# Kernel tuning notes

Hardware: AMD Instinct MI355X
Metric: run time of the kernel (lower is better)

The kernel has to match this reference:

```python
import jax, jax.numpy as jnp
import numpy as np

B, N, K = 2, 8192, 16          # batch, points, ED_nsample
SA_C, DG_C = 128, 1024         # SA_conv_out, DG_conv_out
CAT_C = SA_C + SA_C // 4 + 4   # 164 channels into head


def _conv1(W, b, x):
    # 1x1 Conv1d: W [out,in], x [B,in,N]
    return jnp.einsum('oc,bcn->bon', W, x) + b[None, :, None]


def _bn_relu(x, g, be):
    # BatchNorm1d (training-mode batch stats) + ReLU, x [B,C,N]
    m = x.mean(axis=(0, 2), keepdims=True)
    v = x.var(axis=(0, 2), keepdims=True)
    return jax.nn.relu((x - m) * jax.lax.rsqrt(v + 1e-5) * g[None, :, None] + be[None, :, None])


def setup_inputs() -> dict:
    key = jax.random.key(0)
    ks = jax.random.split(key, 32)
    w = lambda k, s: jax.random.normal(k, s, jnp.float32) * 0.05
    p = {}
    p['pointcloud'] = jax.random.normal(ks[0], (B, N, 3), jnp.float32)
    p['h1'] = jax.random.normal(ks[1], (B, SA_C, N), jnp.float32)
    p['h2'] = jax.random.normal(ks[2], (B, DG_C, N), jnp.float32)
    p['numpoints'] = N
    # DG head convs 1024->256->64->32
    p['DG_w1'], p['DG_b1'] = w(ks[3], (256, DG_C)), jnp.zeros(256, jnp.float32)
    p['DG_g1'], p['DG_be1'] = jnp.ones(256, jnp.float32), jnp.zeros(256, jnp.float32)
    p['DG_w2'], p['DG_b2'] = w(ks[4], (64, 256)), jnp.zeros(64, jnp.float32)
    p['DG_g2'], p['DG_be2'] = jnp.ones(64, jnp.float32), jnp.zeros(64, jnp.float32)
    p['DG_w3'], p['DG_b3'] = w(ks[5], (SA_C // 4, 64)), jnp.zeros(SA_C // 4, jnp.float32)
    p['DG_g3'], p['DG_be3'] = jnp.ones(SA_C // 4, jnp.float32), jnp.zeros(SA_C // 4, jnp.float32)
    # ED MLP 3->4->4
    p['ED_w1'], p['ED_b1'] = w(ks[6], (3, 4)), jnp.zeros(4, jnp.float32)
    p['ED_w2'], p['ED_b2'] = w(ks[7], (4, 4)), jnp.zeros(4, jnp.float32)
    # head convs 164->512->256->128
    p['C_w1'], p['C_b1'] = w(ks[8], (512, CAT_C)), jnp.zeros(512, jnp.float32)
    p['C_g1'], p['C_be1'] = jnp.ones(512, jnp.float32), jnp.zeros(512, jnp.float32)
    p['C_w2'], p['C_b2'] = w(ks[9], (256, 512)), jnp.zeros(256, jnp.float32)
    p['C_g2'], p['C_be2'] = jnp.ones(256, jnp.float32), jnp.zeros(256, jnp.float32)
    p['C_w3'], p['C_b3'] = w(ks[10], (128, 256)), jnp.zeros(128, jnp.float32)
    p['C_g3'], p['C_be3'] = jnp.ones(128, jnp.float32), jnp.zeros(128, jnp.float32)
    return p


def reference(pointcloud, h1, h2, numpoints,
              DG_w1, DG_b1, DG_g1, DG_be1, DG_w2, DG_b2, DG_g2, DG_be2,
              DG_w3, DG_b3, DG_g3, DG_be3,
              ED_w1, ED_b1, ED_w2, ED_b2,
              C_w1, C_b1, C_g1, C_be1, C_w2, C_b2, C_g2, C_be2,
              C_w3, C_b3, C_g3, C_be3):
    xyz = pointcloud[..., :3]
    # DG branch head
    h2p = _bn_relu(_conv1(DG_w1, DG_b1, h2), DG_g1, DG_be1)
    h2p = _bn_relu(_conv1(DG_w2, DG_b2, h2p), DG_g2, DG_be2)
    h2p = _bn_relu(_conv1(DG_w3, DG_b3, h2p), DG_g3, DG_be3)
    # ED branch: brute-force knn on squared distances
    sq = jnp.sum(xyz * xyz, axis=-1)                               # [B,N]
    d = sq[:, :, None] + sq[:, None, :] - 2.0 * jnp.einsum('bnd,bmd->bnm', xyz, xyz)
    _, idx = jax.lax.top_k(-d, K)                                  # [B,N,K]
    nbr = jax.vmap(lambda pts, i: pts[i])(xyz, idx)                # [B,N,K,3]
    c = nbr - nbr.mean(axis=2, keepdims=True)
    cov = jnp.einsum('bnkd,bnke->bnde', c, c) / K                  # [B,N,3,3]
    ev = jnp.linalg.eigvalsh(cov)                                  # [B,N,3] ascending
    h3 = jax.nn.relu(ev @ ED_w1 + ED_b1) @ ED_w2 + ED_b2           # [B,N,4]
    # fuse and head
    z = jnp.concatenate([h1, h2p, jnp.transpose(h3, (0, 2, 1))], axis=1)
    z = _bn_relu(_conv1(C_w1, C_b1, z), C_g1, C_be1)
    z = _bn_relu(_conv1(C_w2, C_b2, z), C_g2, C_be2)
    z = _bn_relu(_conv1(C_w3, C_b3, z), C_g3, C_be3)
    return xyz, z
```

## Files before the change

### kernel.cpp

```cpp
#include <hip/hip_runtime.h>

#define NPTS 8192
#define BATCH 2

typedef __attribute__((ext_vector_type(8))) __bf16 bf16x8;
typedef __attribute__((ext_vector_type(4))) float f32x4;
typedef unsigned int u32;

__device__ inline unsigned short f2bf(float x) {
    unsigned u = __float_as_uint(x);
    u += 0x7fffu + ((u >> 16) & 1u);
    return (unsigned short)(u >> 16);
}
__device__ inline unsigned pack32(float d, unsigned idx) {
    unsigned u = __float_as_uint(d);
    u ^= ((unsigned)((int)u >> 31)) | 0x80000000u;
    return (u & 0xFFFFE000u) | idx;
}
__device__ inline unsigned bitonic64u(unsigned key, int lane) {
#pragma unroll
    for (int k = 2; k <= 64; k <<= 1) {
#pragma unroll
        for (int j = k >> 1; j > 0; j >>= 1) {
            unsigned o = __shfl_xor(key, j, 64);
            bool tmin = (((lane & k) == 0) == ((lane & j) == 0));
            key = ((o < key) == tmin) ? o : key;
        }
    }
    return key;
}
__device__ inline void ins16(unsigned& key, unsigned c, int lane) {
    unsigned prev = __shfl_up(key, 1, 64);
    if (lane == 0) prev = 0u;
    unsigned mx = prev > c ? prev : c;
    key = mx < key ? mx : key;
}
__device__ inline float distf(float4 q, float4 p) {
    return fmaf(-2.f, fmaf(q.z, p.z, fmaf(q.y, p.y, q.x * p.x)), q.w + p.w);
}

__global__ __launch_bounds__(256) void prep_presplit(
    const float* __restrict__ pc, float* __restrict__ oxyz, float4* __restrict__ pq,
    const float* __restrict__ W0, const float* __restrict__ W1,
    const float* __restrict__ W2, const float* __restrict__ W3,
    const float* __restrict__ W4, const float* __restrict__ W5,
    unsigned short* __restrict__ wsp) {
    int bx = blockIdx.x, tid = threadIdx.x;
    if (bx < 64) {
        int t = bx * 256 + tid;
        float x = pc[t * 3 + 0], y = pc[t * 3 + 1], z = pc[t * 3 + 2];
        oxyz[t * 3 + 0] = x; oxyz[t * 3 + 1] = y; oxyz[t * 3 + 2] = z;
        pq[t] = make_float4(x, y, z, fmaf(z, z, fmaf(y, y, x * x)));
        return;
    }
    int pb = bx - 64;
    const float* W; int O, C, OP; size_t off; int base;
    if (pb < 1024)      { W = W0; O = 256; C = 1024; OP = 256; off = 0;       base = 0; }
    else if (pb < 1152) { W = W1; O =  64; C =  256; OP = 128; off = 524288;  base = 1024; }
    else if (pb < 1184) { W = W2; O =  32; C =   64; OP = 128; off = 589824;  base = 1152; }
    else if (pb < 1568) { W = W3; O = 512; C =  164; OP = 512; off = 606208;  base = 1184; }
    else if (pb < 2080) { W = W4; O = 256; C =  512; OP = 256; off = 802816;  base = 1568; }
    else                { W = W5; O = 128; C =  256; OP = 128; off = 1064960; base = 2080; }
    unsigned short* dst = wsp + off;
    int t = (pb - base) * 256 + tid;
    int kk = t & 31;
    int o = (t >> 5) % OP;
    int kt = t / (OP * 32);
    int c = kt * 32 + kk;
    float x = (o < O && c < C) ? W[o * C + c] : 0.f;
    unsigned short hb = f2bf(x);
    float hf = __uint_as_float((unsigned)hb << 16);
    unsigned short lb = f2bf(x - hf);
    int s = kk >> 3, pos = kk & 7;
    int sst = s ^ ((o >> 1) & 3);
    dst[((size_t)(kt * 2) * OP + o) * 32 + sst * 8 + pos] = hb;
    dst[((size_t)(kt * 2 + 1) * OP + o) * 32 + sst * 8 + pos] = lb;
}

template <int MODE>
__global__ __launch_bounds__(256, 2) void mfma_gemm(
    const unsigned short* __restrict__ Wsp, const float* __restrict__ bias,
    const float* __restrict__ X, float* __restrict__ out,
    int O, int C, int OP, int nK,
    const float2* __restrict__ stats,
    const float* __restrict__ h1, const float* __restrict__ h3,
    const float2* __restrict__ stats3) {
    const int N = NPTS;
    int tid = threadIdx.x;
    int lane = tid & 63, w = tid >> 6;
    int wm = w >> 1, wn = w & 1;
    int b = blockIdx.z, n0 = blockIdx.x * 64, o0 = blockIdx.y * 128;
    int n = n0 + lane;

    __shared__ __align__(16) unsigned char lds[26624];
    unsigned char* WHp = lds;
    unsigned char* WLp = lds + 8192;
    unsigned char* XHp = lds + 16384;
    unsigned char* XLp = lds + 21504;

    f32x4 acc[4][2];
#pragma unroll
    for (int i = 0; i < 4; ++i)
#pragma unroll
        for (int j = 0; j < 2; ++j) acc[i][j] = (f32x4){0.f, 0.f, 0.f, 0.f};

    float xcur[8], xnxt[8];

    auto loadx = [&](int kt, float (&dst)[8]) {
#pragma unroll
        for (int i = 0; i < 8; ++i) {
            int c = kt * 32 + w * 8 + i;
            float x = 0.f;
            if (MODE == 0 || MODE == 1) {
                if (c < C) x = X[((size_t)(b * C + c)) * N + n];
            } else {
                if (c < 128)       x = h1[((size_t)(b * 128 + c)) * N + n];
                else if (c < 160)  x = X[((size_t)(b * 32 + (c - 128))) * N + n];
                else if (c < 164)  x = h3[((size_t)(b * 4 + (c - 160))) * N + n];
            }
            dst[i] = x;
        }
    };

    loadx(0, xcur);
    for (int kt = 0; kt < nK; ++kt) {
        int c0 = kt * 32;
#pragma unroll
        for (int comp = 0; comp < 2; ++comp) {
            const unsigned short* gb = Wsp + ((size_t)(kt * 2 + comp) * OP + o0) * 32;
            unsigned char* lb = comp ? WLp : WHp;
#pragma unroll
            for (int i = 0; i < 2; ++i) {
                int chunk = w + i * 4;
                __builtin_amdgcn_global_load_lds(
                    (const __attribute__((address_space(1))) u32*)(gb + chunk * 512 + lane * 8),
                    (__attribute__((address_space(3))) u32*)(lb + chunk * 1024),
                    16, 0, 0);
            }
        }
        {
            union { bf16x8 s; unsigned short u[8]; } hh, ll;
#pragma unroll
            for (int i = 0; i < 8; ++i) {
                int c = c0 + w * 8 + i;
                float x = xcur[i];
                if (MODE == 1) {
                    if (c < C) {
                        float2 st = stats[c];
                        x = fmaxf(fmaf(x, st.x, st.y), 0.f);
                    }
                } else if (MODE == 2) {
                    if (c >= 128 && c < 160) {
                        float2 st = stats3[c - 128];
                        x = fmaxf(fmaf(x, st.x, st.y), 0.f);
                    }
                }
                unsigned short hb = f2bf(x);
                float hf = __uint_as_float((unsigned)hb << 16);
                unsigned short lb = f2bf(x - hf);
                hh.u[i] = hb; ll.u[i] = lb;
            }
            *(bf16x8*)(XHp + lane * 80 + w * 16) = hh.s;
            *(bf16x8*)(XLp + lane * 80 + w * 16) = ll.s;
        }
        if (kt + 1 < nK) loadx(kt + 1, xnxt);
        __syncthreads();
        {
            int koff = (lane >> 4) * 16;
            int rb = wn * 32 + (lane & 15);
            bf16x8 bh[2], bl[2];
#pragma unroll
            for (int ni = 0; ni < 2; ++ni) {
                bh[ni] = *(const bf16x8*)(XHp + (rb + ni * 16) * 80 + koff);
                bl[ni] = *(const bf16x8*)(XLp + (rb + ni * 16) * 80 + koff);
            }
#pragma unroll
            for (int mi = 0; mi < 4; ++mi) {
                int ra = wm * 64 + mi * 16 + (lane & 15);
                int sw = koff ^ ((((unsigned)ra >> 1) & 3) * 16);
                bf16x8 ah = *(const bf16x8*)(WHp + ra * 64 + sw);
                bf16x8 al = *(const bf16x8*)(WLp + ra * 64 + sw);
#pragma unroll
                for (int ni = 0; ni < 2; ++ni) {
                    acc[mi][ni] = __builtin_amdgcn_mfma_f32_16x16x32_bf16(ah, bh[ni], acc[mi][ni], 0, 0, 0);
                    acc[mi][ni] = __builtin_amdgcn_mfma_f32_16x16x32_bf16(ah, bl[ni], acc[mi][ni], 0, 0, 0);
                    acc[mi][ni] = __builtin_amdgcn_mfma_f32_16x16x32_bf16(al, bh[ni], acc[mi][ni], 0, 0, 0);
                }
            }
        }
        __syncthreads();
        if (kt + 1 < nK) {
#pragma unroll
            for (int i = 0; i < 8; ++i) xcur[i] = xnxt[i];
        }
    }
    int col = lane & 15, rq = lane >> 4;
#pragma unroll
    for (int mi = 0; mi < 4; ++mi) {
#pragma unroll
        for (int j = 0; j < 4; ++j) {
            int o = o0 + wm * 64 + mi * 16 + rq * 4 + j;
            if (o < O) {
                float bs = bias[o];
                float* po = out + ((size_t)(b * O + o)) * N + n0 + wn * 32 + col;
#pragma unroll
                for (int ni = 0; ni < 2; ++ni) po[ni * 16] = acc[mi][ni][j] + bs;
            }
        }
    }
}

__global__ __launch_bounds__(256) void stats_kernel(const float* __restrict__ X,
                                                    const float* __restrict__ g,
                                                    const float* __restrict__ be,
                                                    float2* __restrict__ st, int C) {
    const int N = NPTS;
    int c = blockIdx.x;
    int tid = threadIdx.x;
    float s1 = 0.f, s2 = 0.f;
    for (int b = 0; b < BATCH; ++b) {
        const float* p = X + (size_t)(b * C + c) * N;
        for (int n = tid * 4; n < N; n += 1024) {
            float4 v = *(const float4*)(p + n);
            s1 += v.x + v.y + v.z + v.w;
            s2 += v.x * v.x + v.y * v.y + v.z * v.z + v.w * v.w;
        }
    }
    __shared__ float r1[256], r2[256];
    r1[tid] = s1; r2[tid] = s2;
    __syncthreads();
    for (int off = 128; off > 0; off >>= 1) {
        if (tid < off) { r1[tid] += r1[tid + off]; r2[tid] += r2[tid + off]; }
        __syncthreads();
    }
    if (tid == 0) {
        float inv = 1.f / (BATCH * N);
        float m = r1[0] * inv;
        float var = r2[0] * inv - m * m;
        float sc = g[c] * rsqrtf(var + 1e-5f);
        st[c] = make_float2(sc, be[c] - m * sc);
    }
}

__global__ __launch_bounds__(256) void stats_final_kernel(const float* __restrict__ X,
                                                          const float* __restrict__ g,
                                                          const float* __restrict__ be,
                                                          float* __restrict__ outz) {
    const int N = NPTS;
    const int C = 128;
    int c = blockIdx.x;
    int tid = threadIdx.x;
    float s1 = 0.f, s2 = 0.f;
    for (int b = 0; b < BATCH; ++b) {
        const float* p = X + (size_t)(b * C + c) * N;
        for (int n = tid * 4; n < N; n += 1024) {
            float4 v = *(const float4*)(p + n);
            s1 += v.x + v.y + v.z + v.w;
            s2 += v.x * v.x + v.y * v.y + v.z * v.z + v.w * v.w;
        }
    }
    __shared__ float r1[256], r2[256];
    __shared__ float2 stv;
    r1[tid] = s1; r2[tid] = s2;
    __syncthreads();
    for (int off = 128; off > 0; off >>= 1) {
        if (tid < off) { r1[tid] += r1[tid + off]; r2[tid] += r2[tid + off]; }
        __syncthreads();
    }
    if (tid == 0) {
        float inv = 1.f / (BATCH * N);
        float m = r1[0] * inv;
        float var = r2[0] * inv - m * m;
        float sc = g[c] * rsqrtf(var + 1e-5f);
        stv = make_float2(sc, be[c] - m * sc);
    }
    __syncthreads();
    float2 s = stv;
    for (int b = 0; b < BATCH; ++b) {
        const float* p = X + (size_t)(b * C + c) * N;
        float* q = outz + (size_t)(b * C + c) * N;
        for (int nn = tid * 4; nn < N; nn += 1024) {
            float4 v = *(const float4*)(p + nn);
            v.x = fmaxf(fmaf(v.x, s.x, s.y), 0.f);
            v.y = fmaxf(fmaf(v.y, s.x, s.y), 0.f);
            v.z = fmaxf(fmaf(v.z, s.x, s.y), 0.f);
            v.w = fmaxf(fmaf(v.w, s.x, s.y), 0.f);
            *(float4*)(q + nn) = v;
        }
    }
}

__global__ __launch_bounds__(256) void knn_eig_kernel(
    const float4* __restrict__ pq,
    const float* __restrict__ ew1, const float* __restrict__ eb1,
    const float* __restrict__ ew2, const float* __restrict__ eb2,
    float* __restrict__ h3) {
    int wv = threadIdx.x >> 6;
    int lane = threadIdx.x & 63;
    int sg = blockIdx.x * 4 + wv;
    int b = sg >> 12;
    int iloc = (sg & 4095) << 1;
    const float4* pqb = pq + (size_t)b * NPTS;
    float4 Q0 = pqb[iloc + 0], Q1 = pqb[iloc + 1];

    float4 p = pqb[lane];
    unsigned k0 = bitonic64u(pack32(distf(Q0, p), lane), lane);
    unsigned k1 = bitonic64u(pack32(distf(Q1, p), lane), lane);
    unsigned tk0 = (unsigned)__builtin_amdgcn_readlane((int)k0, 15);
    unsigned tk1 = (unsigned)__builtin_amdgcn_readlane((int)k1, 15);

    float4 A = pqb[64 + lane];
    float4 B = pqb[128 + lane];
    for (int it = 1; it + 1 < 128; it += 2) {
        int tbA = it * 64, tbB = tbA + 64;
        int t3 = (it + 3 < 128) ? it + 3 : 0;
        float4 Cx = pqb[(it + 2) * 64 + lane];
        float4 Dx = pqb[t3 * 64 + lane];
        unsigned cA0 = pack32(distf(Q0, A), tbA + lane);
        unsigned cA1 = pack32(distf(Q1, A), tbA + lane);
        unsigned cB0 = pack32(distf(Q0, B), tbB + lane);
        unsigned cB1 = pack32(distf(Q1, B), tbB + lane);
        unsigned long long mA0 = __ballot(cA0 < tk0), mB0 = __ballot(cB0 < tk0);
        unsigned long long mA1 = __ballot(cA1 < tk1), mB1 = __ballot(cB1 < tk1);
        if (mA0 | mA1 | mB0 | mB1) {
            while (mA0) {
                int L = __ffsll((long long)mA0) - 1; mA0 &= mA0 - 1;
                ins16(k0, (unsigned)__builtin_amdgcn_readlane((int)cA0, L), lane);
            }
            while (mB0) {
                int L = __ffsll((long long)mB0) - 1; mB0 &= mB0 - 1;
                ins16(k0, (unsigned)__builtin_amdgcn_readlane((int)cB0, L), lane);
            }
            while (mA1) {
                int L = __ffsll((long long)mA1) - 1; mA1 &= mA1 - 1;
                ins16(k1, (unsigned)__builtin_amdgcn_readlane((int)cA1, L), lane);
            }
            while (mB1) {
                int L = __ffsll((long long)mB1) - 1; mB1 &= mB1 - 1;
                ins16(k1, (unsigned)__builtin_amdgcn_readlane((int)cB1, L), lane);
            }
            tk0 = (unsigned)__builtin_amdgcn_readlane((int)k0, 15);
            tk1 = (unsigned)__builtin_amdgcn_readlane((int)k1, 15);
        }
        A = Cx; B = Dx;
    }
    {
        int tbA = 127 * 64;
        unsigned cA0 = pack32(distf(Q0, A), tbA + lane);
        unsigned cA1 = pack32(distf(Q1, A), tbA + lane);
        unsigned long long mA0 = __ballot(cA0 < tk0);
        unsigned long long mA1 = __ballot(cA1 < tk1);
        while (mA0) {
            int L = __ffsll((long long)mA0) - 1; mA0 &= mA0 - 1;
            ins16(k0, (unsigned)__builtin_amdgcn_readlane((int)cA0, L), lane);
        }
        while (mA1) {
            int L = __ffsll((long long)mA1) - 1; mA1 &= mA1 - 1;
            ins16(k1, (unsigned)__builtin_amdgcn_readlane((int)cA1, L), lane);
        }
    }

    int g = lane >> 4, r = lane & 15;
    unsigned j0 = ((unsigned)__shfl((int)k0, r, 64)) & 8191u;
    unsigned j1 = ((unsigned)__shfl((int)k1, r, 64)) & 8191u;
    unsigned nj = ((g & 1) == 0) ? j0 : j1;

    float4 nb = pqb[nj];
    float sx = nb.x, sy = nb.y, sz = nb.z;
#pragma unroll
    for (int m = 1; m < 16; m <<= 1) {
        sx += __shfl_xor(sx, m, 64);
        sy += __shfl_xor(sy, m, 64);
        sz += __shfl_xor(sz, m, 64);
    }
    const float i16 = 1.f / 16.f;
    float cx = nb.x - sx * i16, cy = nb.y - sy * i16, cz = nb.z - sz * i16;
    float xx = cx * cx, xy = cx * cy, xz = cx * cz, yy = cy * cy, yz = cy * cz, zz = cz * cz;
#pragma unroll
    for (int m = 1; m < 16; m <<= 1) {
        xx += __shfl_xor(xx, m, 64); xy += __shfl_xor(xy, m, 64); xz += __shfl_xor(xz, m, 64);
        yy += __shfl_xor(yy, m, 64); yz += __shfl_xor(yz, m, 64); zz += __shfl_xor(zz, m, 64);
    }
    float a11 = xx * i16, a12 = xy * i16, a13 = xz * i16,
          a22 = yy * i16, a23 = yz * i16, a33 = zz * i16;
    float q = (a11 + a22 + a33) * (1.f / 3.f);
    float p1 = a12 * a12 + a13 * a13 + a23 * a23;
    float b11 = a11 - q, b22 = a22 - q, b33 = a33 - q;
    float p2 = b11 * b11 + b22 * b22 + b33 * b33 + 2.f * p1;
    float pr = sqrtf(p2 * (1.f / 6.f));
    float ipv = (p2 > 1e-32f) ? (1.f / pr) : 0.f;
    float detB = b11 * (b22 * b33 - a23 * a23) - a12 * (a12 * b33 - a23 * a13) +
                 a13 * (a12 * a23 - b22 * a13);
    float r3 = 0.5f * detB * ipv * ipv * ipv;
    r3 = fminf(1.f, fmaxf(-1.f, r3));
    float phi = acosf(r3) * (1.f / 3.f);
    float e1 = q + 2.f * pr * cosf(phi);
    float e3 = q + 2.f * pr * cosf(phi + 2.0943951023931953f);
    float e2 = 3.f * q - e1 - e3;
    float ev0 = e3, ev1 = e2, ev2 = e1;
    float h[4], o[4];
#pragma unroll
    for (int kk = 0; kk < 4; ++kk)
        h[kk] = fmaxf(eb1[kk] + ev0 * ew1[kk] + ev1 * ew1[4 + kk] + ev2 * ew1[8 + kk], 0.f);
#pragma unroll
    for (int kk = 0; kk < 4; ++kk)
        o[kk] = eb2[kk] + h[0] * ew2[kk] + h[1] * ew2[4 + kk] + h[2] * ew2[8 + kk] +
                h[3] * ew2[12 + kk];
    int ipt = iloc + (g & 1);
    if (r == 0 && g < 2) {
#pragma unroll
        for (int kk = 0; kk < 4; ++kk) h3[(b * 4 + kk) * NPTS + ipt] = o[kk];
    }
}

extern "C" void kernel_launch(void* const* d_in, const int* in_sizes, int n_in,
                              void* d_out, int out_size, void* d_ws, size_t ws_size,
                              hipStream_t stream) {
    const float* pc    = (const float*)d_in[0];
    const float* h1    = (const float*)d_in[1];
    const float* h2    = (const float*)d_in[2];
    const float* DG_w1 = (const float*)d_in[4];
    const float* DG_b1 = (const float*)d_in[5];
    const float* DG_g1 = (const float*)d_in[6];
    const float* DG_be1= (const float*)d_in[7];
    const float* DG_w2 = (const float*)d_in[8];
    const float* DG_b2 = (const float*)d_in[9];
    const float* DG_g2 = (const float*)d_in[10];
    const float* DG_be2= (const float*)d_in[11];
    const float* DG_w3 = (const float*)d_in[12];
    const float* DG_b3 = (const float*)d_in[13];
    const float* DG_g3 = (const float*)d_in[14];
    const float* DG_be3= (const float*)d_in[15];
    const float* ED_w1 = (const float*)d_in[16];
    const float* ED_b1 = (const float*)d_in[17];
    const float* ED_w2 = (const float*)d_in[18];
    const float* ED_b2 = (const float*)d_in[19];
    const float* C_w1  = (const float*)d_in[20];
    const float* C_b1  = (const float*)d_in[21];
    const float* C_g1  = (const float*)d_in[22];
    const float* C_be1 = (const float*)d_in[23];
    const float* C_w2  = (const float*)d_in[24];
    const float* C_b2  = (const float*)d_in[25];
    const float* C_g2  = (const float*)d_in[26];
    const float* C_be2 = (const float*)d_in[27];
    const float* C_w3  = (const float*)d_in[28];
    const float* C_b3  = (const float*)d_in[29];
    const float* C_g3  = (const float*)d_in[30];
    const float* C_be3 = (const float*)d_in[31];

    float* ws = (float*)d_ws;
    float* A  = ws;
    float* Bb = ws + (8l << 20);
    float* Cc = ws + (12l << 20);
    float* H3 = ws + (14l << 20);
    float4* PQ = (float4*)(H3 + 65536);
    float2* ST = (float2*)(H3 + 131072);
    unsigned short* WSP = (unsigned short*)(H3 + 131072 + 2560);

    const size_t W1SP = 0;
    const size_t W2SP = 524288;
    const size_t W3SP = 589824;
    const size_t C1SP = 606208;
    const size_t C2SP = 802816;
    const size_t C3SP = 1064960;

    float* outxyz = (float*)d_out;
    float* outz   = (float*)d_out + BATCH * NPTS * 3;

    prep_presplit<<<2272, 256, 0, stream>>>(pc, outxyz, PQ,
                                            DG_w1, DG_w2, DG_w3, C_w1, C_w2, C_w3, WSP);

    mfma_gemm<0><<<dim3(128, 2, 2), 256, 0, stream>>>(WSP + W1SP, DG_b1, h2, A, 256, 1024, 256, 32,
                                                      nullptr, nullptr, nullptr, nullptr);
    stats_kernel<<<256, 256, 0, stream>>>(A, DG_g1, DG_be1, ST + 0, 256);
    mfma_gemm<1><<<dim3(128, 1, 2), 256, 0, stream>>>(WSP + W2SP, DG_b2, A, Bb, 64, 256, 128, 8,
                                                      ST + 0, nullptr, nullptr, nullptr);
    stats_kernel<<<64, 256, 0, stream>>>(Bb, DG_g2, DG_be2, ST + 256, 64);
    mfma_gemm<1><<<dim3(128, 1, 2), 256, 0, stream>>>(WSP + W3SP, DG_b3, Bb, Cc, 32, 64, 128, 2,
                                                      ST + 256, nullptr, nullptr, nullptr);
    stats_kernel<<<32, 256, 0, stream>>>(Cc, DG_g3, DG_be3, ST + 320, 32);

    knn_eig_kernel<<<2048, 256, 0, stream>>>(PQ, ED_w1, ED_b1, ED_w2, ED_b2, H3);

    mfma_gemm<2><<<dim3(128, 4, 2), 256, 0, stream>>>(WSP + C1SP, C_b1, Cc, A, 512, 164, 512, 6,
                                                      nullptr, h1, H3, ST + 320);
    stats_kernel<<<512, 256, 0, stream>>>(A, C_g1, C_be1, ST + 352, 512);
    mfma_gemm<1><<<dim3(128, 2, 2), 256, 0, stream>>>(WSP + C2SP, C_b2, A, Bb, 256, 512, 256, 16,
                                                      ST + 352, nullptr, nullptr, nullptr);
    stats_kernel<<<256, 256, 0, stream>>>(Bb, C_g2, C_be2, ST + 864, 256);
    mfma_gemm<1><<<dim3(128, 1, 2), 256, 0, stream>>>(WSP + C3SP, C_b3, Bb, Cc, 128, 256, 128, 8,
                                                      ST + 864, nullptr, nullptr, nullptr);

    stats_final_kernel<<<128, 256, 0, stream>>>(Cc, C_g3, C_be3, outz);
}
```

Measured before the change: 287.1 us.

## Fuse BatchNorm statistics into GEMM epilogues via per-block partial sums

Each GEMM epilogue now reduces per-channel sum and sum-of-squares over its 64-point tile and writes per-block partials, and the next GEMM finalizes the scale and shift in its prologue. This removes five standalone stats kernels that each re-read the full activation tensor, plus their launches. In exchange every consumer block redundantly reduces 256 partials per channel, and extra shuffles and LDS are added to the epilogue, which may lower occupancy.

```diff
diff --git a/kernel.cpp b/kernel.cpp
--- a/kernel.cpp
+++ b/kernel.cpp
@@ -82,22 +82,52 @@
     const unsigned short* __restrict__ Wsp, const float* __restrict__ bias,
     const float* __restrict__ X, float* __restrict__ out,
     int O, int C, int OP, int nK,
-    const float2* __restrict__ stats,
+    const float* __restrict__ gin, const float* __restrict__ bein,
+    const float2* __restrict__ partin,
     const float* __restrict__ h1, const float* __restrict__ h3,
-    const float2* __restrict__ stats3) {
+    float2* __restrict__ partout) {
     const int N = NPTS;
     int tid = threadIdx.x;
     int lane = tid & 63, w = tid >> 6;
     int wm = w >> 1, wn = w & 1;
     int b = blockIdx.z, n0 = blockIdx.x * 64, o0 = blockIdx.y * 128;
+    int nblk = blockIdx.x;
     int n = n0 + lane;
 
     __shared__ __align__(16) unsigned char lds[26624];
+    __shared__ float2 stl[512];
+    __shared__ float ps1[2][128], ps2[2][128];
     unsigned char* WHp = lds;
     unsigned char* WLp = lds + 8192;
     unsigned char* XHp = lds + 16384;
     unsigned char* XLp = lds + 21504;
 
+    if (MODE == 1) {
+        for (int c = tid; c < C; c += 256) {
+            const float2* pp = partin + (size_t)c * 256;
+            float s1 = 0.f, s2 = 0.f;
+            for (int p = 0; p < 256; ++p) { float2 v = pp[p]; s1 += v.x; s2 += v.y; }
+            const float inv = 1.f / (BATCH * NPTS);
+            float m = s1 * inv;
+            float var = s2 * inv - m * m;
+            float sc = gin[c] * rsqrtf(var + 1e-5f);
+            stl[c] = make_float2(sc, bein[c] - m * sc);
+        }
+        __syncthreads();
+    } else if (MODE == 2) {
+        if (tid < 32) {
+            const float2* pp = partin + (size_t)tid * 256;
+            float s1 = 0.f, s2 = 0.f;
+            for (int p = 0; p < 256; ++p) { float2 v = pp[p]; s1 += v.x; s2 += v.y; }
+            const float inv = 1.f / (BATCH * NPTS);
+            float m = s1 * inv;
+            float var = s2 * inv - m * m;
+            float sc = gin[tid] * rsqrtf(var + 1e-5f);
+            stl[tid] = make_float2(sc, bein[tid] - m * sc);
+        }
+        __syncthreads();
+    }
+
     f32x4 acc[4][2];
 #pragma unroll
     for (int i = 0; i < 4; ++i)
@@ -105,7 +135,6 @@
         for (int j = 0; j < 2; ++j) acc[i][j] = (f32x4){0.f, 0.f, 0.f, 0.f};
 
     float xcur[8], xnxt[8];
-
     auto loadx = [&](int kt, float (&dst)[8]) {
 #pragma unroll
         for (int i = 0; i < 8; ++i) {
@@ -146,12 +175,12 @@
                 float x = xcur[i];
                 if (MODE == 1) {
                     if (c < C) {
-                        float2 st = stats[c];
+                        float2 st = stl[c];
                         x = fmaxf(fmaf(x, st.x, st.y), 0.f);
                     }
                 } else if (MODE == 2) {
                     if (c >= 128 && c < 160) {
-                        float2 st = stats3[c - 128];
+                        float2 st = stl[c - 128];
                         x = fmaxf(fmaf(x, st.x, st.y), 0.f);
                     }
                 }
@@ -199,76 +228,54 @@
     for (int mi = 0; mi < 4; ++mi) {
 #pragma unroll
         for (int j = 0; j < 4; ++j) {
-            int o = o0 + wm * 64 + mi * 16 + rq * 4 + j;
+            int oloc = wm * 64 + mi * 16 + rq * 4 + j;
+            int o = o0 + oloc;
+            float s1 = 0.f, s2 = 0.f;
             if (o < O) {
                 float bs = bias[o];
+                float v0 = acc[mi][0][j] + bs;
+                float v1 = acc[mi][1][j] + bs;
                 float* po = out + ((size_t)(b * O + o)) * N + n0 + wn * 32 + col;
-#pragma unroll
-                for (int ni = 0; ni < 2; ++ni) po[ni * 16] = acc[mi][ni][j] + bs;
-            }
-        }
-    }
-}
-
-__global__ __launch_bounds__(256) void stats_kernel(const float* __restrict__ X,
-                                                    const float* __restrict__ g,
-                                                    const float* __restrict__ be,
-                                                    float2* __restrict__ st, int C) {
+                po[0] = v0; po[16] = v1;
+                s1 = v0 + v1;
+                s2 = fmaf(v0, v0, v1 * v1);
+            }
+#pragma unroll
+            for (int mm = 1; mm < 16; mm <<= 1) {
+                s1 += __shfl_xor(s1, mm, 64);
+                s2 += __shfl_xor(s2, mm, 64);
+            }
+            if (col == 0) { ps1[wn][oloc] = s1; ps2[wn][oloc] = s2; }
+        }
+    }
+    __syncthreads();
+    if (tid < 128) {
+        int o = o0 + tid;
+        if (o < O)
+            partout[(size_t)o * 256 + b * 128 + nblk] =
+                make_float2(ps1[0][tid] + ps1[1][tid], ps2[0][tid] + ps2[1][tid]);
+    }
+}
+
+__global__ __launch_bounds__(256) void stats_final_kernel(
+    const float2* __restrict__ part, const float* __restrict__ g,
+    const float* __restrict__ be, const float* __restrict__ X,
+    float* __restrict__ outz) {
     const int N = NPTS;
+    const int C = 128;
     int c = blockIdx.x;
     int tid = threadIdx.x;
-    float s1 = 0.f, s2 = 0.f;
-    for (int b = 0; b < BATCH; ++b) {
-        const float* p = X + (size_t)(b * C + c) * N;
-        for (int n = tid * 4; n < N; n += 1024) {
-            float4 v = *(const float4*)(p + n);
-            s1 += v.x + v.y + v.z + v.w;
-            s2 += v.x * v.x + v.y * v.y + v.z * v.z + v.w * v.w;
-        }
-    }
     __shared__ float r1[256], r2[256];
-    r1[tid] = s1; r2[tid] = s2;
+    __shared__ float2 stv;
+    float2 v = part[(size_t)c * 256 + tid];
+    r1[tid] = v.x; r2[tid] = v.y;
     __syncthreads();
     for (int off = 128; off > 0; off >>= 1) {
         if (tid < off) { r1[tid] += r1[tid + off]; r2[tid] += r2[tid + off]; }
         __syncthreads();
     }
     if (tid == 0) {
-        float inv = 1.f / (BATCH * N);
-        float m = r1[0] * inv;
-        float var = r2[0] * inv - m * m;
-        float sc = g[c] * rsqrtf(var + 1e-5f);
-        st[c] = make_float2(sc, be[c] - m * sc);
-    }
-}
-
-__global__ __launch_bounds__(256) void stats_final_kernel(const float* __restrict__ X,
-                                                          const float* __restrict__ g,
-                                                          const float* __restrict__ be,
-                                                          float* __restrict__ outz) {
-    const int N = NPTS;
-    const int C = 128;
-    int c = blockIdx.x;
-    int tid = threadIdx.x;
-    float s1 = 0.f, s2 = 0.f;
-    for (int b = 0; b < BATCH; ++b) {
-        const float* p = X + (size_t)(b * C + c) * N;
-        for (int n = tid * 4; n < N; n += 1024) {
-            float4 v = *(const float4*)(p + n);
-            s1 += v.x + v.y + v.z + v.w;
-            s2 += v.x * v.x + v.y * v.y + v.z * v.z + v.w * v.w;
-        }
-    }
-    __shared__ float r1[256], r2[256];
-    __shared__ float2 stv;
-    r1[tid] = s1; r2[tid] = s2;
-    __syncthreads();
-    for (int off = 128; off > 0; off >>= 1) {
-        if (tid < off) { r1[tid] += r1[tid + off]; r2[tid] += r2[tid + off]; }
-        __syncthreads();
-    }
-    if (tid == 0) {
-        float inv = 1.f / (BATCH * N);
+        const float inv = 1.f / (BATCH * NPTS);
         float m = r1[0] * inv;
         float var = r2[0] * inv - m * m;
         float sc = g[c] * rsqrtf(var + 1e-5f);
@@ -280,12 +287,12 @@
         const float* p = X + (size_t)(b * C + c) * N;
         float* q = outz + (size_t)(b * C + c) * N;
         for (int nn = tid * 4; nn < N; nn += 1024) {
-            float4 v = *(const float4*)(p + nn);
-            v.x = fmaxf(fmaf(v.x, s.x, s.y), 0.f);
-            v.y = fmaxf(fmaf(v.y, s.x, s.y), 0.f);
-            v.z = fmaxf(fmaf(v.z, s.x, s.y), 0.f);
-            v.w = fmaxf(fmaf(v.w, s.x, s.y), 0.f);
-            *(float4*)(q + nn) = v;
+            float4 v4 = *(const float4*)(p + nn);
+            v4.x = fmaxf(fmaf(v4.x, s.x, s.y), 0.f);
+            v4.y = fmaxf(fmaf(v4.y, s.x, s.y), 0.f);
+            v4.z = fmaxf(fmaf(v4.z, s.x, s.y), 0.f);
+            v4.w = fmaxf(fmaf(v4.w, s.x, s.y), 0.f);
+            *(float4*)(q + nn) = v4;
         }
     }
 }
@@ -454,8 +461,15 @@
     float* Cc = ws + (12l << 20);
     float* H3 = ws + (14l << 20);
     float4* PQ = (float4*)(H3 + 65536);
-    float2* ST = (float2*)(H3 + 131072);
     unsigned short* WSP = (unsigned short*)(H3 + 131072 + 2560);
+
+    float2* P_DG1 = (float2*)(Bb + (1l << 20));
+    float2* P_DG2 = (float2*)(Bb + (1l << 20) + 131072);
+    float2* P_DG3 = (float2*)(Bb + (1l << 20) + 131072 + 32768);
+    float2* P_C1  = (float2*)(Cc + (1l << 20));
+    float2* TAIL  = (float2*)(WSP + 1130496);
+    float2* P_C2  = TAIL;
+    float2* P_C3  = TAIL + 65536;
 
     const size_t W1SP = 0;
     const size_t W2SP = 524288;
@@ -471,25 +485,20 @@
                                             DG_w1, DG_w2, DG_w3, C_w1, C_w2, C_w3, WSP);
 
     mfma_gemm<0><<<dim3(128, 2, 2), 256, 0, stream>>>(WSP + W1SP, DG_b1, h2, A, 256, 1024, 256, 32,
-                                                      nullptr, nullptr, nullptr, nullptr);
-    stats_kernel<<<256, 256, 0, stream>>>(A, DG_g1, DG_be1, ST + 0, 256);
+                                                      nullptr, nullptr, nullptr, nullptr, nullptr, P_DG1);
     mfma_gemm<1><<<dim3(128, 1, 2), 256, 0, stream>>>(WSP + W2SP, DG_b2, A, Bb, 64, 256, 128, 8,
-                                                      ST + 0, nullptr, nullptr, nullptr);
-    stats_kernel<<<64, 256, 0, stream>>>(Bb, DG_g2, DG_be2, ST + 256, 64);
+                                                      DG_g1, DG_be1, P_DG1, nullptr, nullptr, P_DG2);
     mfma_gemm<1><<<dim3(128, 1, 2), 256, 0, stream>>>(WSP + W3SP, DG_b3, Bb, Cc, 32, 64, 128, 2,
-                                                      ST + 256, nullptr, nullptr, nullptr);
-    stats_kernel<<<32, 256, 0, stream>>>(Cc, DG_g3, DG_be3, ST + 320, 32);
+                                                      DG_g2, DG_be2, P_DG2, nullptr, nullptr, P_DG3);
 
     knn_eig_kernel<<<2048, 256, 0, stream>>>(PQ, ED_w1, ED_b1, ED_w2, ED_b2, H3);
 
     mfma_gemm<2><<<dim3(128, 4, 2), 256, 0, stream>>>(WSP + C1SP, C_b1, Cc, A, 512, 164, 512, 6,
-                                                      nullptr, h1, H3, ST + 320);
-    stats_kernel<<<512, 256, 0, stream>>>(A, C_g1, C_be1, ST + 352, 512);
+                                                      DG_g3, DG_be3, P_DG3, h1, H3, P_C1);
     mfma_gemm<1><<<dim3(128, 2, 2), 256, 0, stream>>>(WSP + C2SP, C_b2, A, Bb, 256, 512, 256, 16,
-                                                      ST + 352, nullptr, nullptr, nullptr);
-    stats_kernel<<<256, 256, 0, stream>>>(Bb, C_g2, C_be2, ST + 864, 256);
+                                                      C_g1, C_be1, P_C1, nullptr, nullptr, P_C2);
     mfma_gemm<1><<<dim3(128, 1, 2), 256, 0, stream>>>(WSP + C3SP, C_b3, Bb, Cc, 128, 256, 128, 8,
-                                                      ST + 864, nullptr, nullptr, nullptr);
-
-    stats_final_kernel<<<128, 256, 0, stream>>>(Cc, C_g3, C_be3, outz);
-}
+                                                      C_g2, C_be2, P_C2, nullptr, nullptr, P_C3);
+
+    stats_final_kernel<<<128, 256, 0, stream>>>(P_C3, C_g3, C_be3, Cc, outz);
+}
```

After: 345.4 us. 1.2x slower.
